# Optimization experiments

Measured on AMD Instinct MI355X. Metric: run time of the kernel, lower is better.

## Reference

```python
import jax, jax.numpy as jnp
import numpy as np

N_QUBITS = 4
N_LAYERS = 2


def _ry_gate(theta):
    # theta: scalar or [B]; returns [2,2] or [B,2,2] complex64
    c, s = jnp.cos(theta / 2), jnp.sin(theta / 2)
    return jnp.stack([jnp.stack([c, -s], -1), jnp.stack([s, c], -1)], -2).astype(jnp.complex64)


def _rz_gate(theta):
    e = jnp.exp(-0.5j * theta.astype(jnp.complex64))
    z = jnp.zeros_like(e)
    return jnp.stack([jnp.stack([e, z], -1), jnp.stack([z, jnp.conj(e)], -1)], -2)


def _apply_1q(state, gate, wire):
    # state: [B,2,2,2,2]; gate: [2,2] (shared) or [B,2,2] (per-sample)
    s = jnp.moveaxis(state, wire + 1, -1)
    if gate.ndim == 3:
        s = jnp.einsum('bij,b...j->b...i', gate, s)
    else:
        s = jnp.einsum('ij,b...j->b...i', gate, s)
    return jnp.moveaxis(s, -1, wire + 1)


def _cnot(state, c, t):
    # flip target axis on the control=1 slice
    ctrl0 = jnp.take(state, 0, axis=c + 1)
    ctrl1 = jnp.take(state, 1, axis=c + 1)
    t_ax = (t + 1) if t < c else t  # target axis after removing control axis
    ctrl1 = jnp.flip(ctrl1, axis=t_ax)
    return jnp.stack([ctrl0, ctrl1], axis=c + 1)


def _circuit(x, weights):
    B = x.shape[0]
    # module: x[:, :n_features] -> tanh * pi -> take first N_QUBITS as angles
    ang = jnp.tanh(x[:, :N_QUBITS]) * jnp.pi  # [B,4]
    state = jnp.zeros((B, 2 ** N_QUBITS), jnp.complex64).at[:, 0].set(1.0)
    state = state.reshape((B,) + (2,) * N_QUBITS)
    # AngleEmbedding (RY per wire, per-sample angles)
    for q in range(N_QUBITS):
        state = _apply_1q(state, _ry_gate(ang[:, q]), q)
    for layer in range(N_LAYERS):
        for q in range(N_QUBITS):
            state = _apply_1q(state, _ry_gate(weights[layer, q, 0]), q)
            state = _apply_1q(state, _rz_gate(weights[layer, q, 1]), q)
        for q in range(N_QUBITS - 1):
            state = _cnot(state, q, q + 1)
        state = _cnot(state, N_QUBITS - 1, 0)
    p = state.real ** 2 + state.imag ** 2  # [B,2,2,2,2]
    zs = []
    for q in range(N_QUBITS):
        other = tuple(a for a in range(1, N_QUBITS + 1) if a != q + 1)
        pq = p.sum(axis=other)  # [B,2]
        zs.append(pq[:, 0] - pq[:, 1])
    return jnp.stack(zs, axis=-1).astype(jnp.float32)  # [B,4]


def setup_inputs() -> dict:
    key = jax.random.key(0)
    k1, k2 = jax.random.split(key)
    x = jax.random.normal(k1, (524288, 8), dtype=jnp.float32)
    weights = jax.random.normal(k2, (N_LAYERS, N_QUBITS, 2), dtype=jnp.float32) * 0.1
    return {"x": x, "weights": weights}


def reference(x, weights):
    return _circuit(x, weights)
```

## Files before the change

### kernel.cpp

```cpp
#include <hip/hip_runtime.h>


#define CNOT_SWAP(cq, tq)                                               \
    {                                                                   \
        const int cm = 8 >> (cq), tm = 8 >> (tq);                       \
        _Pragma("unroll")                                               \
        for (int n = 0; n < 16; ++n)                                    \
            if ((n & cm) && !(n & tm)) {                                \
                int m = n | tm;                                         \
                float tr = re[n]; re[n] = re[m]; re[m] = tr;            \
                float ti = im[n]; im[n] = im[m]; im[m] = ti;            \
            }                                                           \
    }

__global__ __launch_bounds__(256) void qcirc_kernel(
    const float* __restrict__ x, const float* __restrict__ w,
    float* __restrict__ out, int B)
{
    int i = blockIdx.x * blockDim.x + threadIdx.x;
    if (i >= B) return;

    float Wc[4], Ws[4], Zc[4], Zs[4], C1[4], S1[4];
#pragma unroll
    for (int q = 0; q < 4; ++q) {
        float a = 0.5f * w[2 * q];
        Wc[q] = __cosf(a); Ws[q] = __sinf(a);
        float b = 0.5f * w[2 * q + 1];
        Zc[q] = __cosf(b); Zs[q] = __sinf(b);
        float c = 0.5f * w[8 + 2 * q];
        C1[q] = __cosf(c); S1[q] = __sinf(c);
    }

    const float4 xv = *reinterpret_cast<const float4*>(x + (size_t)i * 8);
    float xq[4] = {xv.x, xv.y, xv.z, xv.w};

    float Ar[4][2], Ai[4][2];
#pragma unroll
    for (int q = 0; q < 4; ++q) {
        float e  = __expf(2.f * xq[q]);
        float t  = 1.f - 2.f * __builtin_amdgcn_rcpf(1.f + e);
        float h  = 1.57079632679f * t;
        float cc = __cosf(h), sc = __sinf(h);
        float cq = cc * Wc[q] - sc * Ws[q];
        float sq = sc * Wc[q] + cc * Ws[q];
        Ar[q][0] = cq * Zc[q]; Ai[q][0] = -cq * Zs[q];
        Ar[q][1] = sq * Zc[q]; Ai[q][1] =  sq * Zs[q];
    }

    float t01r[4], t01i[4], t23r[4], t23i[4];
#pragma unroll
    for (int a = 0; a < 2; ++a)
#pragma unroll
        for (int b = 0; b < 2; ++b) {
            int j = a * 2 + b;
            t01r[j] = Ar[0][a] * Ar[1][b] - Ai[0][a] * Ai[1][b];
            t01i[j] = Ar[0][a] * Ai[1][b] + Ai[0][a] * Ar[1][b];
            t23r[j] = Ar[2][a] * Ar[3][b] - Ai[2][a] * Ai[3][b];
            t23i[j] = Ar[2][a] * Ai[3][b] + Ai[2][a] * Ar[3][b];
        }

    float re[16], im[16];
#pragma unroll
    for (int n = 0; n < 16; ++n) {
        int hi = n >> 2, lo = n & 3;
        re[n] = t01r[hi] * t23r[lo] - t01i[hi] * t23i[lo];
        im[n] = t01r[hi] * t23i[lo] + t01i[hi] * t23r[lo];
    }

    CNOT_SWAP(0, 1); CNOT_SWAP(1, 2); CNOT_SWAP(2, 3); CNOT_SWAP(3, 0);

#pragma unroll
    for (int q = 0; q < 4; ++q) {
        const int mask = 8 >> q;
        const float c = C1[q], s = S1[q];
#pragma unroll
        for (int n = 0; n < 16; ++n)
            if (!(n & mask)) {
                int m = n | mask;
                float r0 = re[n], r1 = re[m];
                float i0 = im[n], i1 = im[m];
                re[n] = c * r0 - s * r1;  re[m] = s * r0 + c * r1;
                im[n] = c * i0 - s * i1;  im[m] = s * i0 + c * i1;
            }
    }

    CNOT_SWAP(0, 1); CNOT_SWAP(1, 2); CNOT_SWAP(2, 3); CNOT_SWAP(3, 0);

    float p[16];
#pragma unroll
    for (int n = 0; n < 16; ++n) p[n] = re[n] * re[n] + im[n] * im[n];

    float total = 0.f;
#pragma unroll
    for (int n = 0; n < 16; ++n) total += p[n];

    float z[4];
#pragma unroll
    for (int q = 0; q < 4; ++q) {
        const int mask = 8 >> q;
        float s1 = 0.f;
#pragma unroll
        for (int n = 0; n < 16; ++n)
            if (n & mask) s1 += p[n];
        z[q] = total - 2.f * s1;
    }

    *reinterpret_cast<float4*>(out + (size_t)i * 4) =
        make_float4(z[0], z[1], z[2], z[3]);
}

extern "C" void kernel_launch(void* const* d_in, const int* in_sizes, int n_in,
                              void* d_out, int out_size, void* d_ws, size_t ws_size,
                              hipStream_t stream) {
    const float* x = (const float*)d_in[0];
    const float* w = (const float*)d_in[1];
    float* out = (float*)d_out;
    const int B = in_sizes[0] / 8;
    const int threads = 256;
    const int blocks = (B + threads - 1) / threads;
    hipLaunchKernelGGL(qcirc_kernel, dim3(blocks), dim3(threads), 0, stream,
                       x, w, out, B);
}
```

Before: 71.39 us.

## Replace statevector simulation with closed-form trigonometric polynomial for expectations

The full 16-amplitude complex state simulation is replaced by a precomputed closed-form polynomial in per-sample cos/sin of the combined angle (input angle plus first-layer RY weight). A one-thread setup kernel derives 36 weight-dependent coefficients into the workspace, and the main kernel evaluates each Z expectation as a short FMA chain. This removes most per-thread ALU work and register pressure, but adds a second kernel launch and depends on a hand-derived symbolic expansion that must match the reference for arbitrary weights.

```diff
diff --git a/kernel.cpp b/kernel.cpp
--- a/kernel.cpp
+++ b/kernel.cpp
@@ -1,123 +1,138 @@
 #include <hip/hip_runtime.h>
 
 
-#define CNOT_SWAP(cq, tq)                                               \
-    {                                                                   \
-        const int cm = 8 >> (cq), tm = 8 >> (tq);                       \
-        _Pragma("unroll")                                               \
-        for (int n = 0; n < 16; ++n)                                    \
-            if ((n & cm) && !(n & tm)) {                                \
-                int m = n | tm;                                         \
-                float tr = re[n]; re[n] = re[m]; re[m] = tr;            \
-                float ti = im[n]; im[n] = im[m]; im[m] = ti;            \
-            }                                                           \
+__global__ void qsetup_kernel(const float* __restrict__ w, float* __restrict__ k)
+{
+    if (threadIdx.x != 0) return;
+    float c[4], s[4], cz[4], sz[4];
+#pragma unroll
+    for (int j = 0; j < 4; ++j) {
+        float a1 = w[8 + 2 * j];
+        c[j] = __cosf(a1); s[j] = __sinf(a1);
+        float zz = w[2 * j + 1];
+        cz[j] = __cosf(zz); sz[j] = __sinf(zz);
     }
+    k[0] =  c[1]*c[2]*c[3];
+    k[1] = -c[1]*c[2]*s[3]*cz[0]*cz[1]*cz[3];
+    k[2] =  c[1]*s[2]*c[3]*sz[2]*sz[3];
+    k[3] = -s[1]*c[2]*c[3]*cz[1]*cz[2];
+    k[4] = -c[1]*s[2]*s[3]*sz[0]*sz[1]*cz[2];
+    k[5] = -s[1]*c[2]*s[3]*sz[0]*sz[2]*cz[3];
+    k[6] = -s[1]*s[2]*c[3]*sz[1]*sz[3];
+    k[7] = -s[1]*s[2]*s[3]*cz[0];
+    k[8]  =  c[0]*c[1];
+    k[9]  =  c[0]*s[1]*sz[1]*sz[2];
+    k[10] =  s[0]*c[1]*sz[0]*sz[1];
+    k[11] =  s[0]*s[1]*cz[0]*cz[2];
+    k[12] =  c[0]*c[1]*c[2];
+    k[13] =  c[0]*c[1]*s[2]*sz[2]*sz[3];
+    k[14] = -c[0]*s[1]*c[2]*cz[1]*cz[2];
+    k[15] = -s[0]*c[1]*c[2]*cz[0]*cz[1];
+    k[16] = -c[0]*s[1]*s[2]*sz[1]*sz[3];
+    k[17] = -s[0]*c[1]*s[2]*sz[0]*sz[1]*cz[2]*cz[3];
+    k[18] = -s[0]*s[1]*c[2]*sz[0]*sz[2];
+    k[19] = -s[0]*s[1]*s[2]*cz[0]*cz[3];
+    k[20] =  c[0]*c[1]*c[2]*c[3];
+    k[21] =  c[0]*c[1]*c[2]*s[3]*cz[0]*sz[1]*sz[3];
+    k[22] = -c[0]*c[1]*s[2]*c[3]*cz[2]*cz[3];
+    k[23] =  c[0]*s[1]*c[2]*c[3]*sz[1]*sz[2];
+    k[24] =  s[0]*c[1]*c[2]*c[3]*sz[0]*sz[1];
+    k[25] = -c[0]*c[1]*s[2]*s[3]*sz[0]*cz[1]*sz[2];
+    k[26] = -c[0]*s[1]*c[2]*s[3]*sz[0]*cz[2]*sz[3];
+    k[27] =  c[0]*s[1]*s[2]*c[3]*cz[1]*cz[3];
+    k[28] =  s[0]*c[1]*c[2]*s[3]*cz[3];
+    k[29] = -s[0]*c[1]*s[2]*c[3]*cz[0]*cz[1]*sz[2]*sz[3];
+    k[30] =  s[0]*s[1]*c[2]*c[3]*cz[0]*cz[2];
+    k[31] = -c[0]*s[1]*s[2]*s[3]*cz[0];
+    k[32] = -s[0]*c[1]*s[2]*s[3]*cz[2];
+    k[33] =  s[0]*s[1]*c[2]*s[3]*sz[1]*sz[2]*cz[3];
+    k[34] =  s[0]*s[1]*s[2]*c[3]*sz[0]*sz[3];
+    k[35] =  s[0]*s[1]*s[2]*s[3]*cz[1];
+    k[36] = w[0]; k[37] = w[2]; k[38] = w[4]; k[39] = w[6];
+}
 
-__global__ __launch_bounds__(256) void qcirc_kernel(
-    const float* __restrict__ x, const float* __restrict__ w,
+__global__ __launch_bounds__(256) void qmain_kernel(
+    const float* __restrict__ x, const float* __restrict__ k,
     float* __restrict__ out, int B)
 {
     int i = blockIdx.x * blockDim.x + threadIdx.x;
     if (i >= B) return;
 
-    float Wc[4], Ws[4], Zc[4], Zs[4], C1[4], S1[4];
+    const float4 xv = *reinterpret_cast<const float4*>(x + (size_t)i * 8);
+    const float xq[4] = {xv.x, xv.y, xv.z, xv.w};
+
+    float C[4], S[4];
 #pragma unroll
     for (int q = 0; q < 4; ++q) {
-        float a = 0.5f * w[2 * q];
-        Wc[q] = __cosf(a); Ws[q] = __sinf(a);
-        float b = 0.5f * w[2 * q + 1];
-        Zc[q] = __cosf(b); Zs[q] = __sinf(b);
-        float c = 0.5f * w[8 + 2 * q];
-        C1[q] = __cosf(c); S1[q] = __sinf(c);
+        float e = __expf(2.f * xq[q]);
+        float t = 1.f - 2.f * __builtin_amdgcn_rcpf(1.f + e);
+        float A = fmaf(3.14159265358979f, t, k[36 + q]);
+        C[q] = __cosf(A);
+        S[q] = __sinf(A);
     }
 
-    const float4 xv = *reinterpret_cast<const float4*>(x + (size_t)i * 8);
-    float xq[4] = {xv.x, xv.y, xv.z, xv.w};
+    const float CC = C[0]*C[1], CS = C[0]*S[1], SC = S[0]*C[1], SS = S[0]*S[1];
+    const float cc = C[2]*C[3], cs = C[2]*S[3], sc = S[2]*C[3], ss = S[2]*S[3];
+    const float S1sc = S[1]*sc;
+    const float SSss = SS*ss;
 
-    float Ar[4][2], Ai[4][2];
-#pragma unroll
-    for (int q = 0; q < 4; ++q) {
-        float e  = __expf(2.f * xq[q]);
-        float t  = 1.f - 2.f * __builtin_amdgcn_rcpf(1.f + e);
-        float h  = 1.57079632679f * t;
-        float cc = __cosf(h), sc = __sinf(h);
-        float cq = cc * Wc[q] - sc * Ws[q];
-        float sq = sc * Wc[q] + cc * Ws[q];
-        Ar[q][0] = cq * Zc[q]; Ai[q][0] = -cq * Zs[q];
-        Ar[q][1] = sq * Zc[q]; Ai[q][1] =  sq * Zs[q];
-    }
+    float z0 = k[0] * (CC*C[3]);
+    z0 = fmaf(k[1],  SS*cs,   z0);
+    z0 = fmaf(k[2],  ss,      z0);
+    z0 = fmaf(k[3],  S1sc,    z0);
+    z0 = fmaf(k[4],  SS*S[2], z0);
+    z0 = fmaf(k[5],  SC*ss,   z0);
+    z0 = fmaf(k[6],  CS*cs,   z0);
+    z0 = fmaf(k[7],  S[0],    z0);
 
-    float t01r[4], t01i[4], t23r[4], t23i[4];
-#pragma unroll
-    for (int a = 0; a < 2; ++a)
-#pragma unroll
-        for (int b = 0; b < 2; ++b) {
-            int j = a * 2 + b;
-            t01r[j] = Ar[0][a] * Ar[1][b] - Ai[0][a] * Ai[1][b];
-            t01i[j] = Ar[0][a] * Ai[1][b] + Ai[0][a] * Ar[1][b];
-            t23r[j] = Ar[2][a] * Ar[3][b] - Ai[2][a] * Ai[3][b];
-            t23i[j] = Ar[2][a] * Ai[3][b] + Ai[2][a] * Ar[3][b];
-        }
+    float z1 = k[8] * (C[0]*cc);
+    z1 = fmaf(k[9],  S1sc,      z1);
+    z1 = fmaf(k[10], SS,        z1);
+    z1 = fmaf(k[11], S[0]*S[2], z1);
 
-    float re[16], im[16];
-#pragma unroll
-    for (int n = 0; n < 16; ++n) {
-        int hi = n >> 2, lo = n & 3;
-        re[n] = t01r[hi] * t23r[lo] - t01i[hi] * t23i[lo];
-        im[n] = t01r[hi] * t23i[lo] + t01i[hi] * t23r[lo];
-    }
+    float z2 = k[12] * (C[1]*C[3]);
+    z2 = fmaf(k[13], C[0]*ss,   z2);
+    z2 = fmaf(k[14], CS*sc,     z2);
+    z2 = fmaf(k[15], SS*C[2],   z2);
+    z2 = fmaf(k[16], S[1]*cs,   z2);
+    z2 = fmaf(k[17], SSss,      z2);
+    z2 = fmaf(k[18], SC*S[2],   z2);
+    z2 = fmaf(k[19], S[0]*S[3], z2);
 
-    CNOT_SWAP(0, 1); CNOT_SWAP(1, 2); CNOT_SWAP(2, 3); CNOT_SWAP(3, 0);
+    float z3 = k[20] * (C[0]*C[2]);
+    z3 = fmaf(k[21], SS*S[3],   z3);
+    z3 = fmaf(k[22], C[1]*ss,   z3);
+    z3 = fmaf(k[23], S[1]*S[2], z3);
+    z3 = fmaf(k[24], SS*C[3],   z3);
+    z3 = fmaf(k[25], SS*sc,     z3);
+    z3 = fmaf(k[26], S[0]*ss,   z3);
+    z3 = fmaf(k[27], CS*S[3],   z3);
+    z3 = fmaf(k[28], cs,        z3);
+    z3 = fmaf(k[29], SSss,      z3);
+    z3 = fmaf(k[30], S[0]*sc,   z3);
+    z3 = fmaf(k[31], SC*cc,     z3);
+    z3 = fmaf(k[32], CC*S[2],   z3);
+    z3 = fmaf(k[33], CS*ss,     z3);
+    z3 = fmaf(k[34], SC*cs,     z3);
+    z3 = fmaf(k[35], S[1],      z3);
 
-#pragma unroll
-    for (int q = 0; q < 4; ++q) {
-        const int mask = 8 >> q;
-        const float c = C1[q], s = S1[q];
-#pragma unroll
-        for (int n = 0; n < 16; ++n)
-            if (!(n & mask)) {
-                int m = n | mask;
-                float r0 = re[n], r1 = re[m];
-                float i0 = im[n], i1 = im[m];
-                re[n] = c * r0 - s * r1;  re[m] = s * r0 + c * r1;
-                im[n] = c * i0 - s * i1;  im[m] = s * i0 + c * i1;
-            }
-    }
-
-    CNOT_SWAP(0, 1); CNOT_SWAP(1, 2); CNOT_SWAP(2, 3); CNOT_SWAP(3, 0);
-
-    float p[16];
-#pragma unroll
-    for (int n = 0; n < 16; ++n) p[n] = re[n] * re[n] + im[n] * im[n];
-
-    float total = 0.f;
-#pragma unroll
-    for (int n = 0; n < 16; ++n) total += p[n];
-
-    float z[4];
-#pragma unroll
-    for (int q = 0; q < 4; ++q) {
-        const int mask = 8 >> q;
-        float s1 = 0.f;
-#pragma unroll
-        for (int n = 0; n < 16; ++n)
-            if (n & mask) s1 += p[n];
-        z[q] = total - 2.f * s1;
-    }
-
-    *reinterpret_cast<float4*>(out + (size_t)i * 4) =
-        make_float4(z[0], z[1], z[2], z[3]);
+    *reinterpret_cast<float4*>(out + (size_t)i * 4) = make_float4(z0, z1, z2, z3);
 }
 
 extern "C" void kernel_launch(void* const* d_in, const int* in_sizes, int n_in,
                               void* d_out, int out_size, void* d_ws, size_t ws_size,
-                              hipStream_t stream) {
+                              hipStream_t stream)
+{
     const float* x = (const float*)d_in[0];
     const float* w = (const float*)d_in[1];
     float* out = (float*)d_out;
+    float* k = (float*)d_ws;
     const int B = in_sizes[0] / 8;
+
+    hipLaunchKernelGGL(qsetup_kernel, dim3(1), dim3(64), 0, stream, w, k);
+
     const int threads = 256;
     const int blocks = (B + threads - 1) / threads;
-    hipLaunchKernelGGL(qcirc_kernel, dim3(blocks), dim3(threads), 0, stream,
-                       x, w, out, B);
+    hipLaunchKernelGGL(qmain_kernel, dim3(blocks), dim3(threads), 0, stream,
+                       x, k, out, B);
 }
```

Result: faster. 66.95 us (-6.2%).
